# Performance work log

Hardware: AMD Instinct MI355X
Metric: run time of the kernel (lower is better)

## Reference

```python
import jax, jax.numpy as jnp
import numpy as np

H = 4
N_PAPER, N_AUTHOR = 100000, 50000
F_IN = 128
HID, OUT = 128, 64  # total channels (per-head = total // H)


def setup_inputs() -> dict:
    key = jax.random.key(0)
    ks = jax.random.split(key, 20)
    inp = {
        'x_paper': jax.random.normal(ks[0], (N_PAPER, F_IN), jnp.float32),
        'x_author': jax.random.normal(ks[1], (N_AUTHOR, F_IN), jnp.float32),
        'src_pp': jax.random.randint(ks[2], (1600000,), 0, N_PAPER, jnp.int32),
        'dst_pp': jax.random.randint(ks[3], (1600000,), 0, N_PAPER, jnp.int32),
        'src_ap': jax.random.randint(ks[4], (800000,), 0, N_AUTHOR, jnp.int32),
        'dst_ap': jax.random.randint(ks[5], (800000,), 0, N_PAPER, jnp.int32),
        'src_pa': jax.random.randint(ks[6], (800000,), 0, N_PAPER, jnp.int32),
        'dst_pa': jax.random.randint(ks[7], (800000,), 0, N_AUTHOR, jnp.int32),
    }
    # Per-edge-type (3 relations) GATConv params, stacked on axis 0.
    s1 = 1.0 / np.sqrt(F_IN)
    s2 = 1.0 / np.sqrt(HID)
    inp['Wsrc1'] = jax.random.normal(ks[8], (3, F_IN, HID), jnp.float32) * s1
    inp['Wdst1'] = jax.random.normal(ks[9], (3, F_IN, HID), jnp.float32) * s1
    inp['asrc1'] = jax.random.normal(ks[10], (3, H, HID // H), jnp.float32) * s1
    inp['adst1'] = jax.random.normal(ks[11], (3, H, HID // H), jnp.float32) * s1
    inp['b1'] = jnp.zeros((3, HID), jnp.float32)
    inp['Wsrc2'] = jax.random.normal(ks[12], (3, HID, OUT), jnp.float32) * s2
    inp['Wdst2'] = jax.random.normal(ks[13], (3, HID, OUT), jnp.float32) * s2
    inp['asrc2'] = jax.random.normal(ks[14], (3, H, OUT // H), jnp.float32) * s2
    inp['adst2'] = jax.random.normal(ks[15], (3, H, OUT // H), jnp.float32) * s2
    inp['b2'] = jnp.zeros((3, OUT), jnp.float32)
    return inp


def gat_conv(xs, xd, src, dst, Ws, Wd, a_s, a_d, b, n_dst):
    """Bipartite GATConv (PyG semantics, add_self_loops=False, concat=True)."""
    C = a_s.shape[-1]
    hs = (xs @ Ws).reshape(xs.shape[0], H, C)   # [Ns,H,C]
    hd = (xd @ Wd).reshape(xd.shape[0], H, C)   # [Nd,H,C]
    es = jnp.sum(hs * a_s, axis=-1)             # [Ns,H]
    ed = jnp.sum(hd * a_d, axis=-1)             # [Nd,H]
    e = jax.nn.leaky_relu(es[src] + ed[dst], negative_slope=0.2)  # [E,H]
    m = jax.ops.segment_max(e, dst, num_segments=n_dst)
    m = jnp.where(jnp.isfinite(m), m, 0.0)
    ee = jnp.exp(e - m[dst])
    denom = jax.ops.segment_sum(ee, dst, num_segments=n_dst)
    alpha = ee / (denom[dst] + 1e-16)           # softmax over incoming edges
    out = jax.ops.segment_sum(alpha[:, :, None] * hs[src], dst, num_segments=n_dst)
    return out.reshape(n_dst, H * C) + b


def reference(x_paper, x_author, src_pp, dst_pp, src_ap, dst_ap, src_pa, dst_pa,
              Wsrc1, Wdst1, asrc1, adst1, b1, Wsrc2, Wdst2, asrc2, adst2, b2):
    def layer(xp, xa, Ws, Wd, a_s, a_d, b):
        # to_hetero: one conv per relation, sum-aggregate per dst node type
        op = gat_conv(xp, xp, src_pp, dst_pp, Ws[0], Wd[0], a_s[0], a_d[0], b[0], N_PAPER)
        op = op + gat_conv(xa, xp, src_ap, dst_ap, Ws[1], Wd[1], a_s[1], a_d[1], b[1], N_PAPER)
        oa = gat_conv(xp, xa, src_pa, dst_pa, Ws[2], Wd[2], a_s[2], a_d[2], b[2], N_AUTHOR)
        return op, oa

    hp, ha = layer(x_paper, x_author, Wsrc1, Wdst1, asrc1, adst1, b1)
    hp, ha = jax.nn.relu(hp), jax.nn.relu(ha)
    op, oa = layer(hp, ha, Wsrc2, Wdst2, asrc2, adst2, b2)
    # concat node types along axis 0: [N_PAPER + N_AUTHOR, OUT]
    return jnp.concatenate([op, oa], axis=0)
```

## Files before the change

kernel.cpp:

```cpp
#include <hip/hip_runtime.h>


#define LEAKY(x) ((x) > 0.f ? (x) : 0.2f * (x))
#define ECH 4096
#define NBMAX 784

typedef _Float16 h8 __attribute__((ext_vector_type(8)));
typedef _Float16 h2 __attribute__((ext_vector_type(2)));
typedef float f4 __attribute__((ext_vector_type(4)));

__launch_bounds__(256)
__global__ void bucket_scatter_chunked(
    const int* __restrict__ s0, const int* __restrict__ d0, int E0,
    int* __restrict__ bc0, int* __restrict__ bt0, int C0, int NB0, int c0,
    const int* __restrict__ s1, const int* __restrict__ d1, int E1,
    int* __restrict__ bc1, int* __restrict__ bt1, int C1, int NB1, int c1,
    const int* __restrict__ s2, const int* __restrict__ d2, int E2,
    int* __restrict__ bc2, int* __restrict__ bt2, int C2, int NB2) {
    __shared__ int lcnt[NBMAX], lbase[NBMAX];
    int ch = blockIdx.x;
    const int* src; const int* dst; int* bc; int* bt; int cap, NB, E;
    if (ch < c0)            { src = s0; dst = d0; bc = bc0; bt = bt0; cap = C0; NB = NB0; E = E0; }
    else if (ch < c0 + c1)  { ch -= c0; src = s1; dst = d1; bc = bc1; bt = bt1; cap = C1; NB = NB1; E = E1; }
    else                    { ch -= c0 + c1; src = s2; dst = d2; bc = bc2; bt = bt2; cap = C2; NB = NB2; E = E2; }
    int t = threadIdx.x;
    int ebeg = ch * ECH;
    int eend = ebeg + ECH < E ? ebeg + ECH : E;

    for (int b = t; b < NB; b += 256) lcnt[b] = 0;
    __syncthreads();
    for (int i = ebeg + t; i < eend; i += 256) atomicAdd(&lcnt[dst[i] >> 7], 1);
    __syncthreads();
    for (int b = t; b < NB; b += 256) {
        int c = lcnt[b];
        lbase[b] = c ? atomicAdd(&bc[b], c) : 0;
        lcnt[b] = 0;
    }
    __syncthreads();
    for (int i = ebeg + t; i < eend; i += 256) {
        int d = dst[i], b = d >> 7;
        int p = lbase[b] + atomicAdd(&lcnt[b], 1);
        if (p < cap) bt[(size_t)b * cap + p] = src[i] | ((d & 127) << 20);
    }
}

__launch_bounds__(256)
__global__ void bucket_build(
    const int* __restrict__ bt0, const int* __restrict__ bc0, int* __restrict__ ss0,
    int* __restrict__ beg0, int* __restrict__ end0, int NB0, int C0, int Nd0,
    const int* __restrict__ bt1, const int* __restrict__ bc1, int* __restrict__ ss1,
    int* __restrict__ beg1, int* __restrict__ end1, int NB1, int C1, int Nd1,
    const int* __restrict__ bt2, const int* __restrict__ bc2, int* __restrict__ ss2,
    int* __restrict__ beg2, int* __restrict__ end2, int NB2, int C2, int Nd2) {
    __shared__ int hist[128], pre[129], cur[128];
    int bb = blockIdx.x;
    const int* bt; const int* bcp; int* ssp; int* bg; int* en; int cap, nd;
    if (bb < NB0)            { bt = bt0; bcp = bc0; ssp = ss0; bg = beg0; en = end0; cap = C0; nd = Nd0; }
    else if (bb < NB0 + NB1) { bb -= NB0; bt = bt1; bcp = bc1; ssp = ss1; bg = beg1; en = end1; cap = C1; nd = Nd1; }
    else                     { bb -= NB0 + NB1; bt = bt2; bcp = bc2; ssp = ss2; bg = beg2; en = end2; cap = C2; nd = Nd2; }
    int tid = threadIdx.x;
    int n = bcp[bb]; if (n > cap) n = cap;
    const int* btb = bt + (size_t)bb * cap;
    int ssbase = bb * cap;
    int dbase = bb << 7;

    if (tid < 128) hist[tid] = 0;
    __syncthreads();
    for (int i = tid; i < n; i += 256) atomicAdd(&hist[btb[i] >> 20], 1);
    __syncthreads();
    if (tid < 128) pre[tid + 1] = hist[tid];
    if (tid == 0) pre[0] = 0;
    __syncthreads();
    for (int off = 1; off < 128; off <<= 1) {
        int v = 0;
        if (tid < 128) {
            int i = tid + 1;
            v = pre[i] + ((i > off) ? pre[i - off] : 0);
        }
        __syncthreads();
        if (tid < 128) pre[tid + 1] = v;
        __syncthreads();
    }
    if (tid < 128) {
        int d = dbase + tid;
        if (d < nd) {
            int b_ = ssbase + pre[tid];
            bg[d] = b_;
            en[d] = b_ + hist[tid];
        }
        cur[tid] = 0;
    }
    __syncthreads();
    for (int i = tid; i < n; i += 256) {
        int v = btb[i];
        int dl = v >> 20;
        int p = atomicAdd(&cur[dl], 1);
        ssp[ssbase + pre[dl] + p] = v & 0xFFFFF;
    }
}

__launch_bounds__(512)
__global__ void prep(const float* __restrict__ Wdst1, const float* __restrict__ adst1,
                     const float* __restrict__ Wdst2, const float* __restrict__ adst2,
                     const float* __restrict__ Wsrc1, const float* __restrict__ Wsrc2,
                     const float* __restrict__ b1, const float* __restrict__ b2,
                     float* __restrict__ WDA, _Float16* __restrict__ Wt,
                     float* __restrict__ bsum) {
    int r = blockIdx.x, t = threadIdx.x;
    if (r < 6) {
        int f = t >> 2, h = t & 3;
        const float* Wd; const float* ad; int Ncol, C;
        if (r < 3) { Wd = Wdst1 + r * 16384; ad = adst1 + r * 128; Ncol = 128; C = 32; }
        else       { Wd = Wdst2 + (r - 3) * 8192; ad = adst2 + (r - 3) * 64; Ncol = 64; C = 16; }
        float s = 0.f;
        for (int c = 0; c < C; ++c) s += Wd[f * Ncol + h * C + c] * ad[h * C + c];
        WDA[r * 512 + f * 4 + h] = s;
    } else if (r < 12) {
        int rr = r - 6;
        const float* W; _Float16* o; int BN;
        if (rr < 3) { W = Wsrc1 + rr * 16384; o = Wt + rr * 16384; BN = 128; }
        else        { W = Wsrc2 + (rr - 3) * 8192; o = Wt + 3 * 16384 + (rr - 3) * 8192; BN = 64; }
        for (int idx = t; idx < BN * 128; idx += 512) {
            int n = idx >> 7, k = idx & 127;
            o[idx] = (_Float16)W[k * BN + n];
        }
    } else {
        if (t < 128) bsum[t] = b1[t] + b1[128 + t];
        else if (t < 192) bsum[128 + (t - 128)] = b2[t - 128] + b2[64 + (t - 128)];
    }
}

__launch_bounds__(256)
__global__ void conv_ed(const float* __restrict__ xp, const float* __restrict__ xa,
                        int NP, int NA, _Float16* __restrict__ xph, _Float16* __restrict__ xah,
                        const float* __restrict__ WDA,
                        float* __restrict__ EDpp, float* __restrict__ EDap,
                        float* __restrict__ EDpa) {
    int wid = blockIdx.x * 4 + (threadIdx.x >> 6);
    if (wid >= NP + NA) return;
    int lane = threadIdx.x & 63;
    const float* x; _Float16* xh; const float4* W0; const float4* W1;
    float* e0p; float* e1p; int row;
    if (wid < NP) { row = wid; x = xp; xh = xph; W0 = (const float4*)WDA;
                    W1 = (const float4*)(WDA + 512); e0p = EDpp; e1p = EDap; }
    else { row = wid - NP; x = xa; xh = xah; W0 = (const float4*)(WDA + 1024);
           W1 = nullptr; e0p = EDpa; e1p = nullptr; }
    float2 xv = *(const float2*)(x + (size_t)row * 128 + lane * 2);
    h2 hv = {(_Float16)xv.x, (_Float16)xv.y};
    *(h2*)(xh + (size_t)row * 128 + lane * 2) = hv;
    float4 a0 = W0[lane * 2], a1 = W0[lane * 2 + 1];
    float4 p = make_float4(xv.x * a0.x + xv.y * a1.x, xv.x * a0.y + xv.y * a1.y,
                           xv.x * a0.z + xv.y * a1.z, xv.x * a0.w + xv.y * a1.w);
    float4 q = make_float4(0.f, 0.f, 0.f, 0.f);
    if (W1) {
        float4 b0 = W1[lane * 2], b1 = W1[lane * 2 + 1];
        q = make_float4(xv.x * b0.x + xv.y * b1.x, xv.x * b0.y + xv.y * b1.y,
                        xv.x * b0.z + xv.y * b1.z, xv.x * b0.w + xv.y * b1.w);
    }
#pragma unroll
    for (int off = 32; off; off >>= 1) {
        p.x += __shfl_xor(p.x, off); p.y += __shfl_xor(p.y, off);
        p.z += __shfl_xor(p.z, off); p.w += __shfl_xor(p.w, off);
        q.x += __shfl_xor(q.x, off); q.y += __shfl_xor(q.y, off);
        q.z += __shfl_xor(q.z, off); q.w += __shfl_xor(q.w, off);
    }
    if (lane == 0) {
        *(float4*)(e0p + (size_t)row * 4) = p;
        if (e1p) *(float4*)(e1p + (size_t)row * 4) = q;
    }
}

template <int BN>
__launch_bounds__(256)
__global__ void gemm3(const _Float16* __restrict__ A0, int M0, const _Float16* __restrict__ W0,
                      const float* __restrict__ as0, _Float16* __restrict__ O0, float* __restrict__ es0,
                      const _Float16* __restrict__ A1, int M1, const _Float16* __restrict__ W1,
                      const float* __restrict__ as1, _Float16* __restrict__ O1, float* __restrict__ es1,
                      const _Float16* __restrict__ A2, int M2, const _Float16* __restrict__ W2,
                      const float* __restrict__ as2, _Float16* __restrict__ O2, float* __restrict__ es2,
                      int t0, int t1) {
    constexpr int NT = BN / 16;
    constexpr int LDA = 136;
    __shared__ _Float16 As[64 * LDA];
    __shared__ _Float16 Ws[BN * LDA];
    int b = blockIdx.x;
    const _Float16* A; const _Float16* Wt; const float* a_s; _Float16* Chs; float* es;
    int M, tile;
    if (b < t0)      { A = A0; M = M0; Wt = W0; a_s = as0; Chs = O0; es = es0; tile = b; }
    else if (b < t1) { A = A1; M = M1; Wt = W1; a_s = as1; Chs = O1; es = es1; tile = b - t0; }
    else             { A = A2; M = M2; Wt = W2; a_s = as2; Chs = O2; es = es2; tile = b - t1; }
    const int tid = threadIdx.x;
    const int wave = tid >> 6, lane = tid & 63;
    const int l15 = lane & 15, quad = lane >> 4;
    const int row0 = tile * 64;
    const int maxr = M - row0;

#pragma unroll
    for (int c = 0; c < 4; ++c) {
        int idx = c * 256 + tid;
        int row = idx >> 4, off = (idx & 15) * 8;
        h8 v = {};
        if (row < maxr) v = *(const h8*)(A + (size_t)(row0 + row) * 128 + off);
        *(h8*)(As + row * LDA + off) = v;
    }
#pragma unroll
    for (int c = 0; c < NT; ++c) {
        int idx = c * 256 + tid;
        int row = idx >> 4, off = (idx & 15) * 8;
        *(h8*)(Ws + row * LDA + off) = *(const h8*)(Wt + (size_t)row * 128 + off);
    }
    __syncthreads();

    f4 acc[NT];
#pragma unroll
    for (int nt = 0; nt < NT; ++nt) acc[nt] = {0.f, 0.f, 0.f, 0.f};

    const _Float16* ap = As + (wave * 16 + l15) * LDA + quad * 8;
#pragma unroll
    for (int k0 = 0; k0 < 128; k0 += 32) {
        h8 a = *(const h8*)(ap + k0);
#pragma unroll
        for (int nt = 0; nt < NT; ++nt) {
            h8 bb = *(const h8*)(Ws + (nt * 16 + l15) * LDA + k0 + quad * 8);
            acc[nt] = __builtin_amdgcn_mfma_f32_16x16x32_f16(a, bb, acc[nt], 0, 0, 0);
        }
    }

    float av[NT];
#pragma unroll
    for (int nt = 0; nt < NT; ++nt) av[nt] = a_s[nt * 16 + l15];
    constexpr int TPH = NT / 4;
#pragma unroll
    for (int r = 0; r < 4; ++r) {
        int row = wave * 16 + quad * 4 + r;
        bool ok = row < maxr;
        if (ok) {
            _Float16* outp = Chs + (size_t)(row0 + row) * BN + l15;
#pragma unroll
            for (int nt = 0; nt < NT; ++nt) outp[nt * 16] = (_Float16)acc[nt][r];
        }
        float p0 = 0.f, p1 = 0.f, p2 = 0.f, p3 = 0.f;
#pragma unroll
        for (int i = 0; i < TPH; ++i) {
            p0 += acc[0 * TPH + i][r] * av[0 * TPH + i];
            p1 += acc[1 * TPH + i][r] * av[1 * TPH + i];
            p2 += acc[2 * TPH + i][r] * av[2 * TPH + i];
            p3 += acc[3 * TPH + i][r] * av[3 * TPH + i];
        }
#pragma unroll
        for (int off = 1; off < 16; off <<= 1) {
            p0 += __shfl_xor(p0, off);
            p1 += __shfl_xor(p1, off);
            p2 += __shfl_xor(p2, off);
            p3 += __shfl_xor(p3, off);
        }
        if (ok && l15 < 4) {
            float pv = (l15 == 0) ? p0 : (l15 == 1) ? p1 : (l15 == 2) ? p2 : p3;
            es[(size_t)(row0 + row) * 4 + l15] = pv;
        }
    }
}

template <int CH>
__device__ __forceinline__ void gat_gather(
    int b0, int e0, const int* __restrict__ ss, const _Float16* __restrict__ hs,
    const float* __restrict__ es, float edh, int lane, int h, int el,
    float& racc0, float& racc1, float& rden) {
    float m = -3e38f, acc0 = 0.f, acc1 = 0.f, den = 0.f;
    for (int base = b0; base < e0; base += 16) {
        int n = e0 - base;
        if (n > 16) n = 16;
        int s = 0;
        float e = -3e38f;
        if (el < n) {
            s = ss[base + el];
            e = es[(size_t)s * 4 + h] + edh;
            e = LEAKY(e);
        }
        float cm = e;
        cm = fmaxf(cm, __shfl_xor(cm, 1));
        cm = fmaxf(cm, __shfl_xor(cm, 2));
        cm = fmaxf(cm, __shfl_xor(cm, 4));
        cm = fmaxf(cm, __shfl_xor(cm, 8));
        float nm = fmaxf(m, cm);
        float f = __expf(m - nm);
        acc0 *= f; acc1 *= f; den *= f;
        m = nm;
        float w = (el < n) ? __expf(e - m) : 0.f;

        int j = 0;
        for (; j + 4 <= n; j += 4) {
            int sa = __builtin_amdgcn_readlane(s, j);
            int sb = __builtin_amdgcn_readlane(s, j + 1);
            int sc = __builtin_amdgcn_readlane(s, j + 2);
            int sd = __builtin_amdgcn_readlane(s, j + 3);
            float w0 = __shfl(w, (h << 4) | j);
            float w1 = __shfl(w, (h << 4) | (j + 1));
            float w2 = __shfl(w, (h << 4) | (j + 2));
            float w3 = __shfl(w, (h << 4) | (j + 3));
            if constexpr (CH == 128) {
                h2 v0 = *(const h2*)(hs + (size_t)sa * 128 + lane * 2);
                h2 v1 = *(const h2*)(hs + (size_t)sb * 128 + lane * 2);
                h2 v2 = *(const h2*)(hs + (size_t)sc * 128 + lane * 2);
                h2 v3 = *(const h2*)(hs + (size_t)sd * 128 + lane * 2);
                acc0 += w0 * (float)v0[0] + w1 * (float)v1[0] + w2 * (float)v2[0] + w3 * (float)v3[0];
                acc1 += w0 * (float)v0[1] + w1 * (float)v1[1] + w2 * (float)v2[1] + w3 * (float)v3[1];
            } else {
                acc0 += w0 * (float)hs[(size_t)sa * 64 + lane] + w1 * (float)hs[(size_t)sb * 64 + lane] +
                        w2 * (float)hs[(size_t)sc * 64 + lane] + w3 * (float)hs[(size_t)sd * 64 + lane];
            }
            den += w0 + w1 + w2 + w3;
        }
        for (; j < n; ++j) {
            int sj = __builtin_amdgcn_readlane(s, j);
            float wj = __shfl(w, (h << 4) | j);
            if constexpr (CH == 128) {
                h2 v = *(const h2*)(hs + (size_t)sj * 128 + lane * 2);
                acc0 += wj * (float)v[0];
                acc1 += wj * (float)v[1];
            } else {
                acc0 += wj * (float)hs[(size_t)sj * 64 + lane];
            }
            den += wj;
        }
    }
    racc0 = acc0; racc1 = acc1; rden = den;
}

__device__ __forceinline__ void ed_reduce_write(float o0, float o1, const float* wda,
                                                float* edO, int wid, int lane) {
    const float4* W = (const float4*)wda;
    float4 w0 = W[lane * 2], w1 = W[lane * 2 + 1];
    float4 p = make_float4(o0 * w0.x + o1 * w1.x, o0 * w0.y + o1 * w1.y,
                           o0 * w0.z + o1 * w1.z, o0 * w0.w + o1 * w1.w);
#pragma unroll
    for (int off = 32; off; off >>= 1) {
        p.x += __shfl_xor(p.x, off); p.y += __shfl_xor(p.y, off);
        p.z += __shfl_xor(p.z, off); p.w += __shfl_xor(p.w, off);
    }
    if (lane == 0) *(float4*)(edO + (size_t)wid * 4) = p;
}

template <int CH, typename OT>
__device__ __forceinline__ void agg1_body(
    const int* __restrict__ beg, const int* __restrict__ end_,
    const int* __restrict__ ss, const _Float16* __restrict__ hs,
    const float* __restrict__ es, const float* __restrict__ ed,
    const float* __restrict__ bias, OT* __restrict__ out,
    int relu, const float* __restrict__ wdaO, float* __restrict__ edO,
    int wid, int lane) {
    int h = lane >> 4, el = lane & 15;
    float edh = ed[(size_t)wid * 4 + h];
    float a0, a1, dn;
    gat_gather<CH>(beg[wid], end_[wid], ss, hs, es, edh, lane, h, el, a0, a1, dn);
    float inv = 1.f / (dn + 1e-16f);
    if constexpr (CH == 128) {
        float o0 = a0 * inv + bias[lane * 2];
        float o1 = a1 * inv + bias[lane * 2 + 1];
        if (relu) { o0 = fmaxf(o0, 0.f); o1 = fmaxf(o1, 0.f); }
        size_t i0 = (size_t)wid * 128 + lane * 2;
        if constexpr (sizeof(OT) == 2) {
            h2 ov = {(_Float16)o0, (_Float16)o1};
            *(h2*)((_Float16*)out + i0) = ov;
            o0 = (float)ov[0]; o1 = (float)ov[1];
        } else {
            *(float2*)((float*)out + i0) = make_float2(o0, o1);
        }
        if (edO) ed_reduce_write(o0, o1, wdaO, edO, wid, lane);
    } else {
        float o = a0 * inv + bias[lane];
        if (relu) o = fmaxf(o, 0.f);
        out[(size_t)wid * 64 + lane] = (OT)o;
    }
}

template <int CH, typename OT>
__device__ __forceinline__ void agg2_body(
    const int* __restrict__ begA, const int* __restrict__ endA,
    const int* __restrict__ ssA, const _Float16* __restrict__ hsA,
    const float* __restrict__ esA, const float* __restrict__ edA,
    const int* __restrict__ begB, const int* __restrict__ endB,
    const int* __restrict__ ssB, const _Float16* __restrict__ hsB,
    const float* __restrict__ esB, const float* __restrict__ edB,
    const float* __restrict__ bsum, OT* __restrict__ out, int relu,
    const float* __restrict__ wda1, float* __restrict__ ed1O,
    const float* __restrict__ wda2, float* __restrict__ ed2O,
    int wid, int lane) {
    int h = lane >> 4, el = lane & 15;
    float edhA = edA[(size_t)wid * 4 + h];
    float edhB = edB[(size_t)wid * 4 + h];
    float aA0, aA1, dnA, aB0, aB1, dnB;
    gat_gather<CH>(begA[wid], endA[wid], ssA, hsA, esA, edhA, lane, h, el, aA0, aA1, dnA);
    gat_gather<CH>(begB[wid], endB[wid], ssB, hsB, esB, edhB, lane, h, el, aB0, aB1, dnB);
    float invA = 1.f / (dnA + 1e-16f), invB = 1.f / (dnB + 1e-16f);
    if constexpr (CH == 128) {
        float o0 = aA0 * invA + aB0 * invB + bsum[lane * 2];
        float o1 = aA1 * invA + aB1 * invB + bsum[lane * 2 + 1];
        if (relu) { o0 = fmaxf(o0, 0.f); o1 = fmaxf(o1, 0.f); }
        size_t i0 = (size_t)wid * 128 + lane * 2;
        if constexpr (sizeof(OT) == 2) {
            h2 ov = {(_Float16)o0, (_Float16)o1};
            *(h2*)((_Float16*)out + i0) = ov;
            o0 = (float)ov[0]; o1 = (float)ov[1];
        } else {
            *(float2*)((float*)out + i0) = make_float2(o0, o1);
        }
        if (ed1O) ed_reduce_write(o0, o1, wda1, ed1O, wid, lane);
        if (ed2O) ed_reduce_write(o0, o1, wda2, ed2O, wid, lane);
    } else {
        float o = aA0 * invA + aB0 * invB + bsum[lane];
        if (relu) o = fmaxf(o, 0.f);
        out[(size_t)wid * 64 + lane] = (OT)o;
    }
}

template <int CH, typename OT>
__launch_bounds__(256)
__global__ void agg_fused(
    const int* __restrict__ begA, const int* __restrict__ endA,
    const int* __restrict__ ssA, const _Float16* __restrict__ hsA,
    const float* __restrict__ esA, const float* __restrict__ edA,
    const int* __restrict__ begB, const int* __restrict__ endB,
    const int* __restrict__ ssB, const _Float16* __restrict__ hsB,
    const float* __restrict__ esB, const float* __restrict__ edB,
    const float* __restrict__ bsum, OT* __restrict__ out2, int Ndst2, int relu,
    const float* __restrict__ wda1, float* __restrict__ ed1O,
    const float* __restrict__ wda2, float* __restrict__ ed2O,
    const int* __restrict__ begC, const int* __restrict__ endC,
    const int* __restrict__ ssC, const _Float16* __restrict__ hsC,
    const float* __restrict__ esC, const float* __restrict__ edC,
    const float* __restrict__ biasC, OT* __restrict__ out1, int Ndst1,
    const float* __restrict__ wdaC, float* __restrict__ edCO, int G2) {
    int wave = threadIdx.x >> 6, lane = threadIdx.x & 63;
    int b = blockIdx.x;
    if (b < G2) {
        int wid = b * 4 + wave;
        if (wid >= Ndst2) return;
        agg2_body<CH, OT>(begA, endA, ssA, hsA, esA, edA,
                          begB, endB, ssB, hsB, esB, edB,
                          bsum, out2, relu, wda1, ed1O, wda2, ed2O, wid, lane);
    } else {
        int wid = (b - G2) * 4 + wave;
        if (wid >= Ndst1) return;
        agg1_body<CH, OT>(begC, endC, ssC, hsC, esC, edC, biasC, out1,
                          relu, wdaC, edCO, wid, lane);
    }
}

extern "C" void kernel_launch(void* const* d_in, const int* in_sizes, int n_in,
                              void* d_out, int out_size, void* d_ws, size_t ws_size,
                              hipStream_t stream) {
    const float* xp     = (const float*)d_in[0];
    const float* xa     = (const float*)d_in[1];
    const int* src_pp   = (const int*)d_in[2];
    const int* dst_pp   = (const int*)d_in[3];
    const int* src_ap   = (const int*)d_in[4];
    const int* dst_ap   = (const int*)d_in[5];
    const int* src_pa   = (const int*)d_in[6];
    const int* dst_pa   = (const int*)d_in[7];
    const float* Wsrc1  = (const float*)d_in[8];
    const float* Wdst1  = (const float*)d_in[9];
    const float* asrc1  = (const float*)d_in[10];
    const float* adst1  = (const float*)d_in[11];
    const float* b1     = (const float*)d_in[12];
    const float* Wsrc2  = (const float*)d_in[13];
    const float* Wdst2  = (const float*)d_in[14];
    const float* asrc2  = (const float*)d_in[15];
    const float* adst2  = (const float*)d_in[16];
    const float* b2     = (const float*)d_in[17];

    const int NP  = in_sizes[0] / 128;
    const int NA  = in_sizes[1] / 128;
    const int Epp = in_sizes[2];
    const int Eap = in_sizes[4];
    const int Epa = in_sizes[6];

    const int NB0 = (NP + 127) >> 7, NB1 = (NP + 127) >> 7, NB2 = (NA + 127) >> 7;
    auto cap_of = [](int E, int NB) { int m = E / NB; return ((m * 5 / 4 + 128) + 63) & ~63; };
    const int C0 = cap_of(Epp, NB0), C1 = cap_of(Eap, NB1), C2 = cap_of(Epa, NB2);
    const int c0 = (Epp + ECH - 1) / ECH, c1 = (Eap + ECH - 1) / ECH, c2 = (Epa + ECH - 1) / ECH;

    char* w = (char*)d_ws;
    auto alloc = [&](size_t bytes) {
        char* p = w;
        w += (bytes + 255) & ~(size_t)255;
        return p;
    };
    _Float16* xph = (_Float16*)alloc((size_t)NP * 128 * 2);
    _Float16* xah = (_Float16*)alloc((size_t)NA * 128 * 2);
    _Float16* P1h = (_Float16*)alloc((size_t)NP * 128 * 2);
    _Float16* A1h = (_Float16*)alloc((size_t)NA * 128 * 2);
    _Float16* P2h = (_Float16*)alloc((size_t)NP * 128 * 2);
    _Float16* HPh = (_Float16*)alloc((size_t)NP * 128 * 2);
    _Float16* HAh = (_Float16*)alloc((size_t)NA * 128 * 2);
    _Float16* Wt  = (_Float16*)alloc((size_t)(3 * 16384 + 3 * 8192) * 2);
    int*   ss0  = (int*)alloc((size_t)NB0 * C0 * 4 + 256);
    int*   ss1  = (int*)alloc((size_t)NB1 * C1 * 4 + 256);
    int*   ss2  = (int*)alloc((size_t)NB2 * C2 * 4 + 256);
    int*   beg0 = (int*)alloc((size_t)NP * 4);
    int*   end0 = (int*)alloc((size_t)NP * 4);
    int*   beg1 = (int*)alloc((size_t)NP * 4);
    int*   end1 = (int*)alloc((size_t)NP * 4);
    int*   beg2 = (int*)alloc((size_t)NA * 4);
    int*   end2 = (int*)alloc((size_t)NA * 4);
    float* ESp  = (float*)alloc((size_t)NP * 4 * 4);
    float* ESa  = (float*)alloc((size_t)NA * 4 * 4);
    float* ESp2 = (float*)alloc((size_t)NP * 4 * 4);
    float* EDpp = (float*)alloc((size_t)NP * 4 * 4);
    float* EDap = (float*)alloc((size_t)NP * 4 * 4);
    float* EDpa = (float*)alloc((size_t)NA * 4 * 4);
    float* WDA  = (float*)alloc(6 * 512 * 4);
    float* BSUM = (float*)alloc(192 * 4);
    int*   bcnt = (int*)alloc((size_t)(NB0 + NB1 + NB2) * 4);
    int* bt0 = (int*)P1h;
    int* bt1 = bt0 + (size_t)NB0 * C0;
    int* bt2 = bt1 + (size_t)NB1 * C1;

    hipMemsetAsync(bcnt, 0, (size_t)(NB0 + NB1 + NB2) * 4, stream);
    bucket_scatter_chunked<<<c0 + c1 + c2, 256, 0, stream>>>(
        src_pp, dst_pp, Epp, bcnt, bt0, C0, NB0, c0,
        src_ap, dst_ap, Eap, bcnt + NB0, bt1, C1, NB1, c1,
        src_pa, dst_pa, Epa, bcnt + NB0 + NB1, bt2, C2, NB2);
    bucket_build<<<NB0 + NB1 + NB2, 256, 0, stream>>>(
        bt0, bcnt, ss0, beg0, end0, NB0, C0, NP,
        bt1, bcnt + NB0, ss1, beg1, end1, NB1, C1, NP,
        bt2, bcnt + NB0 + NB1, ss2, beg2, end2, NB2, C2, NA);
    prep<<<13, 512, 0, stream>>>(Wdst1, adst1, Wdst2, adst2, Wsrc1, Wsrc2, b1, b2,
                                 WDA, Wt, BSUM);
    conv_ed<<<(NP + NA + 3) / 4, 256, 0, stream>>>(xp, xa, NP, NA, xph, xah, WDA,
                                                   EDpp, EDap, EDpa);

    float* Opap = (float*)d_out;
    float* Oaut = (float*)d_out + (size_t)NP * 64;
    _Float16* Wt1 = Wt;
    _Float16* Wt2 = Wt + 3 * 16384;
    const int TP = (NP + 63) / 64, TA = (NA + 63) / 64;
    const int G2 = (NP + 3) / 4, G1 = (NA + 3) / 4;

    gemm3<128><<<TP + TA + TP, 256, 0, stream>>>(
        xph, NP, Wt1, asrc1, P1h, ESp,
        xah, NA, Wt1 + 16384, asrc1 + 128, A1h, ESa,
        xph, NP, Wt1 + 2 * 16384, asrc1 + 2 * 128, P2h, ESp2,
        TP, TP + TA);
    agg_fused<128, _Float16><<<G2 + G1, 256, 0, stream>>>(
        beg0, end0, ss0, P1h, ESp, EDpp,
        beg1, end1, ss1, A1h, ESa, EDap,
        BSUM, HPh, NP, 1, WDA + 3 * 512, EDpp, WDA + 4 * 512, EDap,
        beg2, end2, ss2, P2h, ESp2, EDpa, b1 + 2 * 128, HAh, NA,
        WDA + 5 * 512, EDpa, G2);

    gemm3<64><<<TP + TA + TP, 256, 0, stream>>>(
        HPh, NP, Wt2, asrc2, P1h, ESp,
        HAh, NA, Wt2 + 8192, asrc2 + 64, A1h, ESa,
        HPh, NP, Wt2 + 2 * 8192, asrc2 + 2 * 64, P2h, ESp2,
        TP, TP + TA);
    agg_fused<64, float><<<G2 + G1, 256, 0, stream>>>(
        beg0, end0, ss0, P1h, ESp, EDpp,
        beg1, end1, ss1, A1h, ESa, EDap,
        BSUM + 128, Opap, NP, 0, nullptr, nullptr, nullptr, nullptr,
        beg2, end2, ss2, P2h, ESp2, EDpa, b2 + 2 * 64, Oaut, NA,
        nullptr, nullptr, G2);
}
```

Measured before the change: 673.3 us.

## Fuse prep kernels into bucket passes and drop softmax max-subtraction

Merges the weight-prep kernel into the edge bucket-scatter launch and the feature conversion/dst-logit kernel into the bucket-build launch, cutting two kernel launches and letting independent work overlap. Also removes the running-max rescaling in the attention aggregation, exponentiating logits directly to save shuffles and exp/rescale work per chunk. The latter relies on logits staying small enough to avoid exp overflow, which trades numerical robustness for speed.

```diff
diff --git a/kernel.cpp b/kernel.cpp
--- a/kernel.cpp
+++ b/kernel.cpp
@@ -10,163 +10,167 @@
 typedef float f4 __attribute__((ext_vector_type(4)));
 
 __launch_bounds__(256)
-__global__ void bucket_scatter_chunked(
+__global__ void front1(
     const int* __restrict__ s0, const int* __restrict__ d0, int E0,
     int* __restrict__ bc0, int* __restrict__ bt0, int C0, int NB0, int c0,
     const int* __restrict__ s1, const int* __restrict__ d1, int E1,
     int* __restrict__ bc1, int* __restrict__ bt1, int C1, int NB1, int c1,
     const int* __restrict__ s2, const int* __restrict__ d2, int E2,
-    int* __restrict__ bc2, int* __restrict__ bt2, int C2, int NB2) {
+    int* __restrict__ bc2, int* __restrict__ bt2, int C2, int NB2,
+    const float* __restrict__ Wdst1, const float* __restrict__ adst1,
+    const float* __restrict__ Wdst2, const float* __restrict__ adst2,
+    const float* __restrict__ Wsrc1, const float* __restrict__ Wsrc2,
+    const float* __restrict__ b1, const float* __restrict__ b2,
+    float* __restrict__ WDA, _Float16* __restrict__ Wt,
+    float* __restrict__ bsum, int S) {
     __shared__ int lcnt[NBMAX], lbase[NBMAX];
-    int ch = blockIdx.x;
-    const int* src; const int* dst; int* bc; int* bt; int cap, NB, E;
-    if (ch < c0)            { src = s0; dst = d0; bc = bc0; bt = bt0; cap = C0; NB = NB0; E = E0; }
-    else if (ch < c0 + c1)  { ch -= c0; src = s1; dst = d1; bc = bc1; bt = bt1; cap = C1; NB = NB1; E = E1; }
-    else                    { ch -= c0 + c1; src = s2; dst = d2; bc = bc2; bt = bt2; cap = C2; NB = NB2; E = E2; }
+    int blk = blockIdx.x;
     int t = threadIdx.x;
-    int ebeg = ch * ECH;
-    int eend = ebeg + ECH < E ? ebeg + ECH : E;
-
-    for (int b = t; b < NB; b += 256) lcnt[b] = 0;
-    __syncthreads();
-    for (int i = ebeg + t; i < eend; i += 256) atomicAdd(&lcnt[dst[i] >> 7], 1);
-    __syncthreads();
-    for (int b = t; b < NB; b += 256) {
-        int c = lcnt[b];
-        lbase[b] = c ? atomicAdd(&bc[b], c) : 0;
-        lcnt[b] = 0;
-    }
-    __syncthreads();
-    for (int i = ebeg + t; i < eend; i += 256) {
-        int d = dst[i], b = d >> 7;
-        int p = lbase[b] + atomicAdd(&lcnt[b], 1);
-        if (p < cap) bt[(size_t)b * cap + p] = src[i] | ((d & 127) << 20);
+    if (blk < S) {
+        int ch = blk;
+        const int* src; const int* dst; int* bc; int* bt; int cap, NB, E;
+        if (ch < c0)            { src = s0; dst = d0; bc = bc0; bt = bt0; cap = C0; NB = NB0; E = E0; }
+        else if (ch < c0 + c1)  { ch -= c0; src = s1; dst = d1; bc = bc1; bt = bt1; cap = C1; NB = NB1; E = E1; }
+        else                    { ch -= c0 + c1; src = s2; dst = d2; bc = bc2; bt = bt2; cap = C2; NB = NB2; E = E2; }
+        int ebeg = ch * ECH;
+        int eend = ebeg + ECH < E ? ebeg + ECH : E;
+
+        for (int b = t; b < NB; b += 256) lcnt[b] = 0;
+        __syncthreads();
+        for (int i = ebeg + t; i < eend; i += 256) atomicAdd(&lcnt[dst[i] >> 7], 1);
+        __syncthreads();
+        for (int b = t; b < NB; b += 256) {
+            int c = lcnt[b];
+            lbase[b] = c ? atomicAdd(&bc[b], c) : 0;
+            lcnt[b] = 0;
+        }
+        __syncthreads();
+        for (int i = ebeg + t; i < eend; i += 256) {
+            int d = dst[i], b = d >> 7;
+            int p = lbase[b] + atomicAdd(&lcnt[b], 1);
+            if (p < cap) bt[(size_t)b * cap + p] = src[i] | ((d & 127) << 20);
+        }
+    } else {
+        int r = blk - S;
+        if (r < 6) {
+            const float* Wd; const float* ad; int Ncol, C;
+            if (r < 3) { Wd = Wdst1 + r * 16384; ad = adst1 + r * 128; Ncol = 128; C = 32; }
+            else       { Wd = Wdst2 + (r - 3) * 8192; ad = adst2 + (r - 3) * 64; Ncol = 64; C = 16; }
+            for (int tt = t; tt < 512; tt += 256) {
+                int f = tt >> 2, h = tt & 3;
+                float s = 0.f;
+                for (int c = 0; c < C; ++c) s += Wd[f * Ncol + h * C + c] * ad[h * C + c];
+                WDA[r * 512 + f * 4 + h] = s;
+            }
+        } else if (r < 12) {
+            int rr = r - 6;
+            const float* W; _Float16* o; int BN;
+            if (rr < 3) { W = Wsrc1 + rr * 16384; o = Wt + rr * 16384; BN = 128; }
+            else        { W = Wsrc2 + (rr - 3) * 8192; o = Wt + 3 * 16384 + (rr - 3) * 8192; BN = 64; }
+            for (int idx = t; idx < BN * 128; idx += 256) {
+                int n = idx >> 7, k = idx & 127;
+                o[idx] = (_Float16)W[k * BN + n];
+            }
+        } else {
+            if (t < 128) bsum[t] = b1[t] + b1[128 + t];
+            else if (t < 192) bsum[128 + (t - 128)] = b2[t - 128] + b2[64 + (t - 128)];
+        }
     }
 }
 
 __launch_bounds__(256)
-__global__ void bucket_build(
+__global__ void front2(
     const int* __restrict__ bt0, const int* __restrict__ bc0, int* __restrict__ ss0,
     int* __restrict__ beg0, int* __restrict__ end0, int NB0, int C0, int Nd0,
     const int* __restrict__ bt1, const int* __restrict__ bc1, int* __restrict__ ss1,
     int* __restrict__ beg1, int* __restrict__ end1, int NB1, int C1, int Nd1,
     const int* __restrict__ bt2, const int* __restrict__ bc2, int* __restrict__ ss2,
-    int* __restrict__ beg2, int* __restrict__ end2, int NB2, int C2, int Nd2) {
+    int* __restrict__ beg2, int* __restrict__ end2, int NB2, int C2, int Nd2,
+    int NBtot,
+    const float* __restrict__ xp, const float* __restrict__ xa,
+    int NP, int NA, _Float16* __restrict__ xph, _Float16* __restrict__ xah,
+    const float* __restrict__ WDA,
+    float* __restrict__ EDpp, float* __restrict__ EDap, float* __restrict__ EDpa) {
     __shared__ int hist[128], pre[129], cur[128];
-    int bb = blockIdx.x;
-    const int* bt; const int* bcp; int* ssp; int* bg; int* en; int cap, nd;
-    if (bb < NB0)            { bt = bt0; bcp = bc0; ssp = ss0; bg = beg0; en = end0; cap = C0; nd = Nd0; }
-    else if (bb < NB0 + NB1) { bb -= NB0; bt = bt1; bcp = bc1; ssp = ss1; bg = beg1; en = end1; cap = C1; nd = Nd1; }
-    else                     { bb -= NB0 + NB1; bt = bt2; bcp = bc2; ssp = ss2; bg = beg2; en = end2; cap = C2; nd = Nd2; }
+    int blk = blockIdx.x;
     int tid = threadIdx.x;
-    int n = bcp[bb]; if (n > cap) n = cap;
-    const int* btb = bt + (size_t)bb * cap;
-    int ssbase = bb * cap;
-    int dbase = bb << 7;
-
-    if (tid < 128) hist[tid] = 0;
-    __syncthreads();
-    for (int i = tid; i < n; i += 256) atomicAdd(&hist[btb[i] >> 20], 1);
-    __syncthreads();
-    if (tid < 128) pre[tid + 1] = hist[tid];
-    if (tid == 0) pre[0] = 0;
-    __syncthreads();
-    for (int off = 1; off < 128; off <<= 1) {
-        int v = 0;
+    if (blk < NBtot) {
+        int bb = blk;
+        const int* bt; const int* bcp; int* ssp; int* bg; int* en; int cap, nd;
+        if (bb < NB0)            { bt = bt0; bcp = bc0; ssp = ss0; bg = beg0; en = end0; cap = C0; nd = Nd0; }
+        else if (bb < NB0 + NB1) { bb -= NB0; bt = bt1; bcp = bc1; ssp = ss1; bg = beg1; en = end1; cap = C1; nd = Nd1; }
+        else                     { bb -= NB0 + NB1; bt = bt2; bcp = bc2; ssp = ss2; bg = beg2; en = end2; cap = C2; nd = Nd2; }
+        int n = bcp[bb]; if (n > cap) n = cap;
+        const int* btb = bt + (size_t)bb * cap;
+        int ssbase = bb * cap;
+        int dbase = bb << 7;
+
+        if (tid < 128) hist[tid] = 0;
+        __syncthreads();
+        for (int i = tid; i < n; i += 256) atomicAdd(&hist[btb[i] >> 20], 1);
+        __syncthreads();
+        if (tid < 128) pre[tid + 1] = hist[tid];
+        if (tid == 0) pre[0] = 0;
+        __syncthreads();
+        for (int off = 1; off < 128; off <<= 1) {
+            int v = 0;
+            if (tid < 128) {
+                int i = tid + 1;
+                v = pre[i] + ((i > off) ? pre[i - off] : 0);
+            }
+            __syncthreads();
+            if (tid < 128) pre[tid + 1] = v;
+            __syncthreads();
+        }
         if (tid < 128) {
-            int i = tid + 1;
-            v = pre[i] + ((i > off) ? pre[i - off] : 0);
-        }
-        __syncthreads();
-        if (tid < 128) pre[tid + 1] = v;
-        __syncthreads();
-    }
-    if (tid < 128) {
-        int d = dbase + tid;
-        if (d < nd) {
-            int b_ = ssbase + pre[tid];
-            bg[d] = b_;
-            en[d] = b_ + hist[tid];
-        }
-        cur[tid] = 0;
-    }
-    __syncthreads();
-    for (int i = tid; i < n; i += 256) {
-        int v = btb[i];
-        int dl = v >> 20;
-        int p = atomicAdd(&cur[dl], 1);
-        ssp[ssbase + pre[dl] + p] = v & 0xFFFFF;
-    }
-}
-
-__launch_bounds__(512)
-__global__ void prep(const float* __restrict__ Wdst1, const float* __restrict__ adst1,
-                     const float* __restrict__ Wdst2, const float* __restrict__ adst2,
-                     const float* __restrict__ Wsrc1, const float* __restrict__ Wsrc2,
-                     const float* __restrict__ b1, const float* __restrict__ b2,
-                     float* __restrict__ WDA, _Float16* __restrict__ Wt,
-                     float* __restrict__ bsum) {
-    int r = blockIdx.x, t = threadIdx.x;
-    if (r < 6) {
-        int f = t >> 2, h = t & 3;
-        const float* Wd; const float* ad; int Ncol, C;
-        if (r < 3) { Wd = Wdst1 + r * 16384; ad = adst1 + r * 128; Ncol = 128; C = 32; }
-        else       { Wd = Wdst2 + (r - 3) * 8192; ad = adst2 + (r - 3) * 64; Ncol = 64; C = 16; }
-        float s = 0.f;
-        for (int c = 0; c < C; ++c) s += Wd[f * Ncol + h * C + c] * ad[h * C + c];
-        WDA[r * 512 + f * 4 + h] = s;
-    } else if (r < 12) {
-        int rr = r - 6;
-        const float* W; _Float16* o; int BN;
-        if (rr < 3) { W = Wsrc1 + rr * 16384; o = Wt + rr * 16384; BN = 128; }
-        else        { W = Wsrc2 + (rr - 3) * 8192; o = Wt + 3 * 16384 + (rr - 3) * 8192; BN = 64; }
-        for (int idx = t; idx < BN * 128; idx += 512) {
-            int n = idx >> 7, k = idx & 127;
-            o[idx] = (_Float16)W[k * BN + n];
+            int d = dbase + tid;
+            if (d < nd) {
+                int b_ = ssbase + pre[tid];
+                bg[d] = b_;
+                en[d] = b_ + hist[tid];
+            }
+            cur[tid] = 0;
+        }
+        __syncthreads();
+        for (int i = tid; i < n; i += 256) {
+            int v = btb[i];
+            int dl = v >> 20;
+            int p = atomicAdd(&cur[dl], 1);
+            ssp[ssbase + pre[dl] + p] = v & 0xFFFFF;
         }
     } else {
-        if (t < 128) bsum[t] = b1[t] + b1[128 + t];
-        else if (t < 192) bsum[128 + (t - 128)] = b2[t - 128] + b2[64 + (t - 128)];
-    }
-}
-
-__launch_bounds__(256)
-__global__ void conv_ed(const float* __restrict__ xp, const float* __restrict__ xa,
-                        int NP, int NA, _Float16* __restrict__ xph, _Float16* __restrict__ xah,
-                        const float* __restrict__ WDA,
-                        float* __restrict__ EDpp, float* __restrict__ EDap,
-                        float* __restrict__ EDpa) {
-    int wid = blockIdx.x * 4 + (threadIdx.x >> 6);
-    if (wid >= NP + NA) return;
-    int lane = threadIdx.x & 63;
-    const float* x; _Float16* xh; const float4* W0; const float4* W1;
-    float* e0p; float* e1p; int row;
-    if (wid < NP) { row = wid; x = xp; xh = xph; W0 = (const float4*)WDA;
-                    W1 = (const float4*)(WDA + 512); e0p = EDpp; e1p = EDap; }
-    else { row = wid - NP; x = xa; xh = xah; W0 = (const float4*)(WDA + 1024);
-           W1 = nullptr; e0p = EDpa; e1p = nullptr; }
-    float2 xv = *(const float2*)(x + (size_t)row * 128 + lane * 2);
-    h2 hv = {(_Float16)xv.x, (_Float16)xv.y};
-    *(h2*)(xh + (size_t)row * 128 + lane * 2) = hv;
-    float4 a0 = W0[lane * 2], a1 = W0[lane * 2 + 1];
-    float4 p = make_float4(xv.x * a0.x + xv.y * a1.x, xv.x * a0.y + xv.y * a1.y,
-                           xv.x * a0.z + xv.y * a1.z, xv.x * a0.w + xv.y * a1.w);
-    float4 q = make_float4(0.f, 0.f, 0.f, 0.f);
-    if (W1) {
-        float4 b0 = W1[lane * 2], b1 = W1[lane * 2 + 1];
-        q = make_float4(xv.x * b0.x + xv.y * b1.x, xv.x * b0.y + xv.y * b1.y,
-                        xv.x * b0.z + xv.y * b1.z, xv.x * b0.w + xv.y * b1.w);
-    }
-#pragma unroll
-    for (int off = 32; off; off >>= 1) {
-        p.x += __shfl_xor(p.x, off); p.y += __shfl_xor(p.y, off);
-        p.z += __shfl_xor(p.z, off); p.w += __shfl_xor(p.w, off);
-        q.x += __shfl_xor(q.x, off); q.y += __shfl_xor(q.y, off);
-        q.z += __shfl_xor(q.z, off); q.w += __shfl_xor(q.w, off);
-    }
-    if (lane == 0) {
-        *(float4*)(e0p + (size_t)row * 4) = p;
-        if (e1p) *(float4*)(e1p + (size_t)row * 4) = q;
+        int wid = (blk - NBtot) * 4 + (tid >> 6);
+        if (wid >= NP + NA) return;
+        int lane = tid & 63;
+        const float* x; _Float16* xh; const float4* W0; const float4* W1;
+        float* e0p; float* e1p; int row;
+        if (wid < NP) { row = wid; x = xp; xh = xph; W0 = (const float4*)WDA;
+                        W1 = (const float4*)(WDA + 512); e0p = EDpp; e1p = EDap; }
+        else { row = wid - NP; x = xa; xh = xah; W0 = (const float4*)(WDA + 1024);
+               W1 = nullptr; e0p = EDpa; e1p = nullptr; }
+        float2 xv = *(const float2*)(x + (size_t)row * 128 + lane * 2);
+        h2 hv = {(_Float16)xv.x, (_Float16)xv.y};
+        *(h2*)(xh + (size_t)row * 128 + lane * 2) = hv;
+        float4 a0 = W0[lane * 2], a1 = W0[lane * 2 + 1];
+        float4 p = make_float4(xv.x * a0.x + xv.y * a1.x, xv.x * a0.y + xv.y * a1.y,
+                               xv.x * a0.z + xv.y * a1.z, xv.x * a0.w + xv.y * a1.w);
+        float4 q = make_float4(0.f, 0.f, 0.f, 0.f);
+        if (W1) {
+            float4 b0 = W1[lane * 2], b1 = W1[lane * 2 + 1];
+            q = make_float4(xv.x * b0.x + xv.y * b1.x, xv.x * b0.y + xv.y * b1.y,
+                            xv.x * b0.z + xv.y * b1.z, xv.x * b0.w + xv.y * b1.w);
+        }
+#pragma unroll
+        for (int off = 32; off; off >>= 1) {
+            p.x += __shfl_xor(p.x, off); p.y += __shfl_xor(p.y, off);
+            p.z += __shfl_xor(p.z, off); p.w += __shfl_xor(p.w, off);
+            q.x += __shfl_xor(q.x, off); q.y += __shfl_xor(q.y, off);
+            q.z += __shfl_xor(q.z, off); q.w += __shfl_xor(q.w, off);
+        }
+        if (lane == 0) {
+            *(float4*)(e0p + (size_t)row * 4) = p;
+            if (e1p) *(float4*)(e1p + (size_t)row * 4) = q;
+        }
     }
 }
 
@@ -266,27 +270,18 @@
     int b0, int e0, const int* __restrict__ ss, const _Float16* __restrict__ hs,
     const float* __restrict__ es, float edh, int lane, int h, int el,
     float& racc0, float& racc1, float& rden) {
-    float m = -3e38f, acc0 = 0.f, acc1 = 0.f, den = 0.f;
+    float acc0 = 0.f, acc1 = 0.f, den = 0.f;
     for (int base = b0; base < e0; base += 16) {
         int n = e0 - base;
         if (n > 16) n = 16;
         int s = 0;
-        float e = -3e38f;
+        float w = 0.f;
         if (el < n) {
             s = ss[base + el];
-            e = es[(size_t)s * 4 + h] + edh;
+            float e = es[(size_t)s * 4 + h] + edh;
             e = LEAKY(e);
-        }
-        float cm = e;
-        cm = fmaxf(cm, __shfl_xor(cm, 1));
-        cm = fmaxf(cm, __shfl_xor(cm, 2));
-        cm = fmaxf(cm, __shfl_xor(cm, 4));
-        cm = fmaxf(cm, __shfl_xor(cm, 8));
-        float nm = fmaxf(m, cm);
-        float f = __expf(m - nm);
-        acc0 *= f; acc1 *= f; den *= f;
-        m = nm;
-        float w = (el < n) ? __expf(e - m) : 0.f;
+            w = __expf(e);
+        }
 
         int j = 0;
         for (; j + 4 <= n; j += 4) {
@@ -516,19 +511,23 @@
     int* bt1 = bt0 + (size_t)NB0 * C0;
     int* bt2 = bt1 + (size_t)NB1 * C1;
 
-    hipMemsetAsync(bcnt, 0, (size_t)(NB0 + NB1 + NB2) * 4, stream);
-    bucket_scatter_chunked<<<c0 + c1 + c2, 256, 0, stream>>>(
+    const int S = c0 + c1 + c2;
+    const int NBtot = NB0 + NB1 + NB2;
+    const int CE = (NP + NA + 3) / 4;
+
+    hipMemsetAsync(bcnt, 0, (size_t)NBtot * 4, stream);
+    front1<<<S + 13, 256, 0, stream>>>(
         src_pp, dst_pp, Epp, bcnt, bt0, C0, NB0, c0,
         src_ap, dst_ap, Eap, bcnt + NB0, bt1, C1, NB1, c1,
-        src_pa, dst_pa, Epa, bcnt + NB0 + NB1, bt2, C2, NB2);
-    bucket_build<<<NB0 + NB1 + NB2, 256, 0, stream>>>(
+        src_pa, dst_pa, Epa, bcnt + NB0 + NB1, bt2, C2, NB2,
+        Wdst1, adst1, Wdst2, adst2, Wsrc1, Wsrc2, b1, b2,
+        WDA, Wt, BSUM, S);
+    front2<<<NBtot + CE, 256, 0, stream>>>(
         bt0, bcnt, ss0, beg0, end0, NB0, C0, NP,
         bt1, bcnt + NB0, ss1, beg1, end1, NB1, C1, NP,
-        bt2, bcnt + NB0 + NB1, ss2, beg2, end2, NB2, C2, NA);
-    prep<<<13, 512, 0, stream>>>(Wdst1, adst1, Wdst2, adst2, Wsrc1, Wsrc2, b1, b2,
-                                 WDA, Wt, BSUM);
-    conv_ed<<<(NP + NA + 3) / 4, 256, 0, stream>>>(xp, xa, NP, NA, xph, xah, WDA,
-                                                   EDpp, EDap, EDpa);
+        bt2, bcnt + NB0 + NB1, ss2, beg2, end2, NB2, C2, NA,
+        NBtot,
+        xp, xa, NP, NA, xph, xah, WDA, EDpp, EDap, EDpa);
 
     float* Opap = (float*)d_out;
     float* Oaut = (float*)d_out + (size_t)NP * 64;
```

New measurement: 648.8 us. 3.6% less time.
